# Optimization experiments

Hardware: AMD Instinct MI355X
Metric: run time of the kernel (lower is better)

## Reference

```python
import jax, jax.numpy as jnp
import numpy as np

H, D, K, FF = 8, 512, 64, 64  # n_head, feature_dim, key_feature_dim, dim_feedforward
L, B = 512, 32
LN_EPS = 1e-5


def _l2norm(x, eps=1e-12):
    # torch F.normalize: x / max(||x||, eps)
    n = jnp.sqrt(jnp.sum(x * x, axis=-1, keepdims=True))
    return x / jnp.maximum(n, eps)


def _layernorm(x, g, b, eps=LN_EPS):
    m = jnp.mean(x, axis=-1, keepdims=True)
    v = jnp.mean((x - m) ** 2, axis=-1, keepdims=True)
    return (x - m) * jax.lax.rsqrt(v + eps) * g + b


def setup_inputs() -> dict:
    key0 = jax.random.key(0)
    ks = jax.random.split(key0, 13)
    n = jax.random.normal
    s_kq = float(np.sqrt(2.0 / K))
    s_v = float(np.sqrt(2.0 / D))
    return {
        "query": n(ks[0], (L, B, D), jnp.float32),
        "key": n(ks[1], (L, B, D), jnp.float32),
        "value": n(ks[2], (L, B, D), jnp.float32),
        "WK": n(ks[3], (H, K, D), jnp.float32) * s_kq,
        "WQ": n(ks[4], (H, K, D), jnp.float32) * s_kq,
        "WV": n(ks[5], (H, D, D), jnp.float32) * s_v,
        "Wt": n(ks[6], (H, D, D), jnp.float32) * 0.04,  # trans_conv (default kaiming-ish scale)
        "W1": n(ks[7], (H, FF, D), jnp.float32) * 0.04,
        "b1": jnp.zeros((H, FF), jnp.float32),
        "W2": n(ks[8], (H, D, FF), jnp.float32) * 0.1,
        "b2": jnp.zeros((H, D), jnp.float32),
        "ln_g": jnp.ones((H, D), jnp.float32),
        "ln_b": jnp.zeros((H, D), jnp.float32),
    }


def reference(query, key, value, WK, WQ, WV, Wt, W1, b1, W2, b2, ln_g, ln_b):
    # query/key/value: [L, B, D]; per-head weights stacked on leading H axis.
    Lq, Bb, Dd = query.shape
    Hh = WK.shape[0]

    # per-head cosine-normalized Q/K projections: [H, B, L, K]
    wq = _l2norm(jnp.einsum('lbd,hkd->hblk', query, WQ))
    wk = _l2norm(jnp.einsum('lbd,hkd->hblk', key, WK))

    # attention scores [H, B, Lq, Lk], temp = 1
    dot = jnp.einsum('hbqc,hbkc->hbqk', wq, wk)
    aff = jax.nn.softmax(dot, axis=-1)
    # custom renorm: divide by column sums over the QUERY axis
    aff = aff / (1e-9 + jnp.sum(aff, axis=2, keepdims=True))

    wv = jnp.einsum('lbd,hed->hble', value, WV)        # [H, B, Lk, D]
    out = jnp.einsum('hbqk,hbke->hbqe', aff, wv)       # [H, B, Lq, D]
    out = jnp.transpose(out, (0, 2, 1, 3))             # [H, L, B, D]

    # residual-style trans_conv(query - out) -> relu
    o = jax.nn.relu(jnp.einsum('hlbd,hed->hlbe', query[None] - out, Wt))

    # TransNonlinear FFN (dropout = identity at eval)
    hff = jax.nn.relu(jnp.einsum('hlbd,hfd->hlbf', o, W1) + b1[:, None, None, :])
    s2 = jnp.einsum('hlbf,hdf->hlbd', hff, W2) + b2[:, None, None, :]
    x = _layernorm(o + s2, ln_g[:, None, None, :], ln_b[:, None, None, :])

    # concat heads on last dim, head 0 first: [L, B, H*D]
    return jnp.transpose(x, (1, 2, 0, 3)).reshape(Lq, Bb, Hh * Dd)
```

## Files before the change

### kernel.cpp

```cpp
#include <hip/hip_runtime.h>
#include <stdint.h>

#define HH 8
#define DDIM 512
#define KHEAD 64
#define FFD 64
#define LLEN 512
#define BBATCH 32
#define NTOK 16384

typedef unsigned short u16;
typedef __attribute__((ext_vector_type(8))) __bf16 bf16x8;
typedef __attribute__((ext_vector_type(4))) float f32x4;

__device__ __forceinline__ float bf2f(u16 u) {
    union { uint32_t i; float f; } v; v.i = ((uint32_t)u) << 16; return v.f;
}
__device__ __forceinline__ u16 f2bf(float f) {
    union { uint32_t i; float f; } v; v.f = f;
    return (u16)((v.i + 0x7FFFu + ((v.i >> 16) & 1u)) >> 16);
}

__device__ __forceinline__ void gload16(const void* g, void* l) {
    __builtin_amdgcn_global_load_lds(
        (const __attribute__((address_space(1))) void*)g,
        (__attribute__((address_space(3))) void*)l, 16, 0, 0);
}

__global__ __launch_bounds__(256) void f2bf4(const float* __restrict__ in,
                                             u16* __restrict__ out, int n4) {
    int i = blockIdx.x * 256 + threadIdx.x;
    if (i >= n4) return;
    float4 v = ((const float4*)in)[i];
    ushort4 o; o.x = f2bf(v.x); o.y = f2bf(v.y); o.z = f2bf(v.z); o.w = f2bf(v.w);
    ((ushort4*)out)[i] = o;
}

enum { M_PLAIN = 0, M_WQK = 1, M_SUBAUX = 2, M_RELU = 3, M_ADDAUX = 4, M_SCALECOL = 5 };

template<int BM, int BN, int MODE, int ZMAP, int SWAPXY>
__global__ __launch_bounds__(256) void mgemm(
    const u16* __restrict__ A, const u16* __restrict__ B, u16* __restrict__ C,
    int Kd, int lda, int ldb, int ldc,
    long Ash, long Asb, long Bsh, long Bsb, long Csh, long Csb, int nB2,
    const float* __restrict__ bias, int biasN,
    const void* __restrict__ auxp, long auxsh, long auxsb, int auxld)
{
    constexpr int WC = (BN == 128) ? 2 : 1;
    constexpr int WR = 4 / WC;
    constexpr int WTM = BM / WR;
    constexpr int WTN = BN / WC;
    constexpr int MF = WTM / 16;
    constexpr int NF = WTN / 16;
    constexpr int NCA = (BM * 64) / 4096;
    constexpr int NCB = (BN * 64) / 4096;
    __shared__ u16 As[BM * 32];
    __shared__ u16 Bs[BN * 32];

    const int z = blockIdx.z;
    int h2, b2;
    if (ZMAP == 0)      { h2 = z / nB2;      b2 = z % nB2; }
    else if (ZMAP == 1) { h2 = z & 7;        b2 = z >> 3; }
    else                { h2 = (z >> 3) & 7; b2 = ((z >> 6) << 3) | (z & 7); }
    const u16* Ab = A + h2 * Ash + b2 * Asb;
    const u16* Bb = B + h2 * Bsh + b2 * Bsb;
    const int bx = SWAPXY ? blockIdx.y : blockIdx.x;
    const int by = SWAPXY ? blockIdx.x : blockIdx.y;
    const int m0 = bx * BM, n0 = by * BN;
    const int t = threadIdx.x;
    const int lane = t & 63;
    const int w = t >> 6;
    const int wr = w / WC, wc = w % WC;
    const int tb = t * 16;
    const int wb = (t & 192) * 16;

    f32x4 acc[MF][NF];
    #pragma unroll
    for (int m = 0; m < MF; ++m)
        #pragma unroll
        for (int n = 0; n < NF; ++n)
            #pragma unroll
            for (int i = 0; i < 4; ++i) acc[m][n][i] = 0.f;

    const int ko = (lane >> 4) * 16;

    for (int k0 = 0; k0 < Kd; k0 += 32) {
        #pragma unroll
        for (int c = 0; c < NCA; ++c) {
            const int byte = c * 4096 + tb;
            const int row = byte >> 6;
            gload16((const char*)(Ab + (long)(m0 + row) * lda + k0) + (byte & 63),
                    (char*)As + c * 4096 + wb);
        }
        #pragma unroll
        for (int c = 0; c < NCB; ++c) {
            const int byte = c * 4096 + tb;
            const int row = byte >> 6;
            gload16((const char*)(Bb + (long)(n0 + row) * ldb + k0) + (byte & 63),
                    (char*)Bs + c * 4096 + wb);
        }
        __syncthreads();
        bf16x8 af[MF], bfr[NF];
        #pragma unroll
        for (int m = 0; m < MF; ++m)
            af[m] = *(const bf16x8*)((const char*)As + (wr * WTM + m * 16 + (lane & 15)) * 64 + ko);
        #pragma unroll
        for (int n = 0; n < NF; ++n)
            bfr[n] = *(const bf16x8*)((const char*)Bs + (wc * WTN + n * 16 + (lane & 15)) * 64 + ko);
        #pragma unroll
        for (int m = 0; m < MF; ++m)
            #pragma unroll
            for (int n = 0; n < NF; ++n)
                acc[m][n] = __builtin_amdgcn_mfma_f32_16x16x32_bf16(af[m], bfr[n], acc[m][n], 0, 0, 0);
        __syncthreads();
    }

    const int lr = (lane >> 4) * 4;
    const int lc = lane & 15;

    if constexpr (MODE == M_WQK) {
        const int h = (n0 + wc * WTN) >> 6;
        #pragma unroll
        for (int m = 0; m < MF; ++m) {
            #pragma unroll
            for (int i = 0; i < 4; ++i) {
                float s = 0.f;
                #pragma unroll
                for (int n = 0; n < NF; ++n) { const float v = acc[m][n][i]; s += v * v; }
                s += __shfl_xor(s, 1); s += __shfl_xor(s, 2);
                s += __shfl_xor(s, 4); s += __shfl_xor(s, 8);
                const float inv = 1.0f / fmaxf(sqrtf(s), 1e-12f);
                const int r = m0 + wr * WTM + m * 16 + lr + i;
                const int l = r >> 5, bq = r & 31;
                const int sw = (l & 7) << 3;
                u16* rowp = C + (((long)(h * BBATCH + bq) * LLEN + l) * KHEAD);
                #pragma unroll
                for (int n = 0; n < NF; ++n)
                    rowp[(lc + n * 16) ^ sw] = f2bf(acc[m][n][i] * inv);
            }
        }
    } else {
        const long cof = h2 * Csh + b2 * Csb;
        #pragma unroll
        for (int m = 0; m < MF; ++m) {
            #pragma unroll
            for (int i = 0; i < 4; ++i) {
                const int r = m0 + wr * WTM + m * 16 + lr + i;
                #pragma unroll
                for (int n = 0; n < NF; ++n) {
                    const int c = n0 + wc * WTN + n * 16 + lc;
                    float v = acc[m][n][i];
                    if (MODE == M_SUBAUX) {
                        const u16* q = (const u16*)auxp;
                        v = bf2f(q[auxsh * h2 + auxsb * b2 + (long)r * auxld + c]) - v;
                    } else if (MODE == M_RELU) {
                        if (bias) v += bias[h2 * biasN + c];
                        v = fmaxf(v, 0.0f);
                    } else if (MODE == M_ADDAUX) {
                        v += bias[h2 * biasN + c];
                        const u16* ax = (const u16*)auxp;
                        v += bf2f(ax[auxsh * h2 + auxsb * b2 + (long)r * auxld + c]);
                    } else if (MODE == M_SCALECOL) {
                        const float* cs = (const float*)auxp + auxsh * h2 + auxsb * b2;
                        v *= 1.0f / (1e-9f + cs[c]);
                    }
                    C[cof + (long)r * ldc + c] = f2bf(v);
                }
            }
        }
    }
}

__global__ __launch_bounds__(256) void attn_mfma(
    const u16* __restrict__ wq, const u16* __restrict__ wk,
    u16* __restrict__ P, float* __restrict__ colsum)
{
    __shared__ u16 qs[64 * 64];
    __shared__ u16 ks[512 * 64];
    __shared__ float smax[4][64];
    __shared__ float ssum[4][64];

    const int qt = blockIdx.x, b = blockIdx.y, h = blockIdx.z;
    const long hb = h * BBATCH + b;
    const int t = threadIdx.x;
    const int lane = t & 63, w = t >> 6;
    const int wb = (t & 192) * 16;

    const char* qg = (const char*)(wq + (hb * LLEN + qt * 64) * KHEAD);
    const char* kg = (const char*)(wk + hb * LLEN * KHEAD);
    #pragma unroll
    for (int c = 0; c < 2; ++c)
        gload16(qg + c * 4096 + t * 16, (char*)qs + c * 4096 + wb);
    #pragma unroll
    for (int c = 0; c < 16; ++c)
        gload16(kg + c * 4096 + t * 16, (char*)ks + c * 4096 + wb);
    __syncthreads();

    const int l15 = lane & 15;
    const int g = lane >> 4;
    const int swz = (lane & 7) << 4;

    f32x4 acc[4][8];
    #pragma unroll
    for (int m = 0; m < 4; ++m)
        #pragma unroll
        for (int n = 0; n < 8; ++n)
            #pragma unroll
            for (int i = 0; i < 4; ++i) acc[m][n][i] = 0.f;

    #pragma unroll
    for (int kk = 0; kk < 2; ++kk) {
        bf16x8 af[4];
        #pragma unroll
        for (int m = 0; m < 4; ++m) {
            const int row = m * 16 + l15;
            af[m] = *(const bf16x8*)((const char*)qs + row * 128 + ((g * 16 + kk * 64) ^ swz));
        }
        #pragma unroll
        for (int n = 0; n < 8; ++n) {
            const int row = (w * 8 + n) * 16 + l15;
            const bf16x8 bfr = *(const bf16x8*)((const char*)ks + row * 128 + ((g * 16 + kk * 64) ^ swz));
            #pragma unroll
            for (int m = 0; m < 4; ++m)
                acc[m][n] = __builtin_amdgcn_mfma_f32_16x16x32_bf16(af[m], bfr, acc[m][n], 0, 0, 0);
        }
    }

    float rmax[4][4];
    #pragma unroll
    for (int m = 0; m < 4; ++m)
        #pragma unroll
        for (int i = 0; i < 4; ++i) {
            float mx = acc[m][0][i];
            #pragma unroll
            for (int n = 1; n < 8; ++n) mx = fmaxf(mx, acc[m][n][i]);
            mx = fmaxf(mx, __shfl_xor(mx, 1));
            mx = fmaxf(mx, __shfl_xor(mx, 2));
            mx = fmaxf(mx, __shfl_xor(mx, 4));
            mx = fmaxf(mx, __shfl_xor(mx, 8));
            if (l15 == 0) smax[w][m * 16 + g * 4 + i] = mx;
        }
    __syncthreads();
    #pragma unroll
    for (int m = 0; m < 4; ++m)
        #pragma unroll
        for (int i = 0; i < 4; ++i) {
            const int r = m * 16 + g * 4 + i;
            rmax[m][i] = fmaxf(fmaxf(smax[0][r], smax[1][r]),
                               fmaxf(smax[2][r], smax[3][r]));
        }
    float rinv[4][4];
    #pragma unroll
    for (int m = 0; m < 4; ++m)
        #pragma unroll
        for (int i = 0; i < 4; ++i) {
            float s = 0.f;
            #pragma unroll
            for (int n = 0; n < 8; ++n) {
                acc[m][n][i] = __expf(acc[m][n][i] - rmax[m][i]);
                s += acc[m][n][i];
            }
            s += __shfl_xor(s, 1); s += __shfl_xor(s, 2);
            s += __shfl_xor(s, 4); s += __shfl_xor(s, 8);
            if (l15 == 0) ssum[w][m * 16 + g * 4 + i] = s;
        }
    __syncthreads();
    #pragma unroll
    for (int m = 0; m < 4; ++m)
        #pragma unroll
        for (int i = 0; i < 4; ++i) {
            const int r = m * 16 + g * 4 + i;
            rinv[m][i] = 1.0f / (ssum[0][r] + ssum[1][r] + ssum[2][r] + ssum[3][r]);
        }

    u16* Pb = P + (hb * LLEN + qt * 64) * LLEN + w * 128;
    float cs[8];
    #pragma unroll
    for (int n = 0; n < 8; ++n) cs[n] = 0.f;
    #pragma unroll
    for (int m = 0; m < 4; ++m)
        #pragma unroll
        for (int i = 0; i < 4; ++i) {
            const int r = m * 16 + g * 4 + i;
            u16* pr = Pb + (long)r * LLEN + l15;
            const float iv = rinv[m][i];
            #pragma unroll
            for (int n = 0; n < 8; ++n) {
                const float p = acc[m][n][i] * iv;
                pr[n * 16] = f2bf(p);
                cs[n] += p;
            }
        }
    #pragma unroll
    for (int n = 0; n < 8; ++n) {
        cs[n] += __shfl_xor(cs[n], 16);
        cs[n] += __shfl_xor(cs[n], 32);
    }
    if (lane < 16) {
        float* cb = colsum + hb * 512 + w * 128 + lane;
        #pragma unroll
        for (int n = 0; n < 8; ++n) atomicAdd(&cb[n * 16], cs[n]);
    }
}

__global__ __launch_bounds__(256) void ln_out(
    const u16* __restrict__ x, const float* __restrict__ g,
    const float* __restrict__ bb, float* __restrict__ out)
{
    const int t = threadIdx.x;
    const int w = t >> 6, lane = t & 63;
    const long row = (long)blockIdx.x * 4 + w;
    const int h = (int)(row >> 14);
    const int t2 = (int)(row & 16383);
    const int b = t2 >> 9, l = t2 & 511;
    const u16* xp = x + row * DDIM;
    float v[8];
    float s = 0.f, sq = 0.f;
    #pragma unroll
    for (int j = 0; j < 8; ++j) {
        v[j] = bf2f(xp[j * 64 + lane]);
        s += v[j]; sq += v[j] * v[j];
    }
    #pragma unroll
    for (int off = 32; off >= 1; off >>= 1) {
        s += __shfl_xor(s, off);
        sq += __shfl_xor(sq, off);
    }
    const float mean = s * (1.0f / 512.0f);
    const float var = sq * (1.0f / 512.0f) - mean * mean;
    const float rs = rsqrtf(var + 1e-5f);
    const float* gp = g + h * DDIM;
    const float* bp = bb + h * DDIM;
    float* op = out + ((long)l * BBATCH + b) * (HH * DDIM) + h * DDIM;
    #pragma unroll
    for (int j = 0; j < 8; ++j) {
        const int d = j * 64 + lane;
        op[d] = (v[j] - mean) * rs * gp[d] + bp[d];
    }
}

extern "C" void kernel_launch(void* const* d_in, const int* in_sizes, int n_in,
                              void* d_out, int out_size, void* d_ws, size_t ws_size,
                              hipStream_t stream) {
    const float* query = (const float*)d_in[0];
    const float* key   = (const float*)d_in[1];
    const float* value = (const float*)d_in[2];
    const float* WK = (const float*)d_in[3];
    const float* WQ = (const float*)d_in[4];
    const float* WV = (const float*)d_in[5];
    const float* Wt = (const float*)d_in[6];
    const float* W1 = (const float*)d_in[7];
    const float* b1 = (const float*)d_in[8];
    const float* W2 = (const float*)d_in[9];
    const float* b2 = (const float*)d_in[10];
    const float* lng = (const float*)d_in[11];
    const float* lnb = (const float*)d_in[12];

    char* ws = (char*)d_ws;
    u16* kbf  = (u16*)(ws);
    u16* WQbf = (u16*)(ws + 16777216);
    u16* WKbf = (u16*)(ws + 17301504);
    u16* P    = (u16*)(ws);
    u16* preLN = P;
    u16* vbf  = (u16*)(ws + 134217728);
    u16* WVbf = (u16*)(ws + 150994944);
    u16* o    = (u16*)(ws + 134217728);
    float* colsum = (float*)(ws + 268435456);
    u16* qbf  = (u16*)(ws + 268959744);
    u16* hff  = qbf;
    u16* wq   = (u16*)(ws + 285736960);
    u16* wk   = (u16*)(ws + 302514176);
    u16* Wtbf = (u16*)(ws + 285736960);
    u16* W1bf = (u16*)(ws + 289931264);
    u16* W2bf = (u16*)(ws + 290455552);
    u16* qmo = (u16*)d_out;
    u16* wvT = (u16*)((char*)d_out + 134217728);

    if (ws_size < 319291392u) return;

    hipMemsetAsync(colsum, 0, 524288, stream);
    const dim3 blk(256);

    f2bf4<<<dim3(8192), blk, 0, stream>>>(query, qbf, 2097152);
    f2bf4<<<dim3(8192), blk, 0, stream>>>(key,   kbf, 2097152);
    f2bf4<<<dim3(8192), blk, 0, stream>>>(value, vbf, 2097152);
    f2bf4<<<dim3(256),  blk, 0, stream>>>(WQ, WQbf, 65536);
    f2bf4<<<dim3(256),  blk, 0, stream>>>(WK, WKbf, 65536);
    f2bf4<<<dim3(2048), blk, 0, stream>>>(WV, WVbf, 524288);

    mgemm<128, 128, M_WQK, 0, 1><<<dim3(4, 128, 1), blk, 0, stream>>>(
        qbf, WQbf, wq, 512, 512, 512, 0,
        0, 0, 0, 0, 0, 0, 1, nullptr, 0, nullptr, 0, 0, 0);
    mgemm<128, 128, M_WQK, 0, 1><<<dim3(4, 128, 1), blk, 0, stream>>>(
        kbf, WKbf, wk, 512, 512, 512, 0,
        0, 0, 0, 0, 0, 0, 1, nullptr, 0, nullptr, 0, 0, 0);

    attn_mfma<<<dim3(8, 32, 8), blk, 0, stream>>>(wq, wk, P, colsum);

    f2bf4<<<dim3(2048), blk, 0, stream>>>(Wt, Wtbf, 524288);
    f2bf4<<<dim3(256),  blk, 0, stream>>>(W1, W1bf, 65536);
    f2bf4<<<dim3(256),  blk, 0, stream>>>(W2, W2bf, 65536);

    mgemm<128, 128, M_SCALECOL, 2, 0><<<dim3(4, 4, 256), blk, 0, stream>>>(
        WVbf, vbf, wvT, 512, 512, BBATCH * DDIM, 512,
        (long)DDIM * DDIM, 0, 0, DDIM,
        (long)BBATCH * DDIM * LLEN, (long)DDIM * LLEN, 32,
        nullptr, 0, colsum, (long)BBATCH * 512, 512, 0);

    mgemm<128, 128, M_SUBAUX, 1, 0><<<dim3(4, 4, 256), blk, 0, stream>>>(
        P, wvT, qmo, 512, 512, 512, 512,
        (long)BBATCH * LLEN * LLEN, (long)LLEN * LLEN,
        (long)BBATCH * DDIM * LLEN, (long)DDIM * LLEN,
        (long)BBATCH * LLEN * DDIM, (long)LLEN * DDIM, 32,
        nullptr, 0, qbf, 0, DDIM, BBATCH * DDIM);

    mgemm<128, 128, M_RELU, 0, 1><<<dim3(4, 128, 8), blk, 0, stream>>>(
        qmo, Wtbf, o, 512, 512, 512, 512,
        (long)NTOK * DDIM, 0, (long)DDIM * DDIM, 0,
        (long)NTOK * DDIM, 0, 1, nullptr, 512, nullptr, 0, 0, 0);

    mgemm<128, 64, M_RELU, 0, 0><<<dim3(128, 1, 8), blk, 0, stream>>>(
        o, W1bf, hff, 512, 512, 512, 64,
        (long)NTOK * DDIM, 0, (long)FFD * DDIM, 0,
        (long)NTOK * FFD, 0, 1, b1, 64, nullptr, 0, 0, 0);

    mgemm<128, 128, M_ADDAUX, 0, 1><<<dim3(4, 128, 8), blk, 0, stream>>>(
        hff, W2bf, preLN, 64, 64, 64, 512,
        (long)NTOK * FFD, 0, (long)DDIM * FFD, 0,
        (long)NTOK * DDIM, 0, 1, b2, 512, o, (long)NTOK * DDIM, 0, 512);

    ln_out<<<dim3(32768), blk, 0, stream>>>(preLN, lng, lnb, (float*)d_out);
}
```

Baseline: 803.4 us.

## Double-buffer GEMM LDS tiles and fuse FFN second GEMM with LayerNorm

The generic GEMM now keeps two LDS buffers and issues the next K-slice's global-to-LDS loads before computing on the current one, aiming to hide load latency behind MFMA work. The W2 projection, bias, residual add and LayerNorm are merged into one kernel. It keeps W2 for a head in LDS and reduces row statistics across waves, which removes the bf16 preLN round-trip and a separate launch. In exchange the kernels use more LDS (64KB W2 tile plus double buffers), which may lower occupancy. The fused kernel also reads the residual from global memory with an uncoalesced per-fragment pattern.

```diff
diff --git a/kernel.cpp b/kernel.cpp
--- a/kernel.cpp
+++ b/kernel.cpp
@@ -54,8 +54,8 @@
     constexpr int NF = WTN / 16;
     constexpr int NCA = (BM * 64) / 4096;
     constexpr int NCB = (BN * 64) / 4096;
-    __shared__ u16 As[BM * 32];
-    __shared__ u16 Bs[BN * 32];
+    __shared__ u16 As[2][BM * 32];
+    __shared__ u16 Bs[2][BN * 32];
 
     const int z = blockIdx.z;
     int h2, b2;
@@ -84,35 +84,43 @@
 
     const int ko = (lane >> 4) * 16;
 
-    for (int k0 = 0; k0 < Kd; k0 += 32) {
+    auto stage = [&](int buf, int k0) {
         #pragma unroll
         for (int c = 0; c < NCA; ++c) {
             const int byte = c * 4096 + tb;
             const int row = byte >> 6;
             gload16((const char*)(Ab + (long)(m0 + row) * lda + k0) + (byte & 63),
-                    (char*)As + c * 4096 + wb);
+                    (char*)As[buf] + c * 4096 + wb);
         }
         #pragma unroll
         for (int c = 0; c < NCB; ++c) {
             const int byte = c * 4096 + tb;
             const int row = byte >> 6;
             gload16((const char*)(Bb + (long)(n0 + row) * ldb + k0) + (byte & 63),
-                    (char*)Bs + c * 4096 + wb);
-        }
-        __syncthreads();
+                    (char*)Bs[buf] + c * 4096 + wb);
+        }
+    };
+
+    stage(0, 0);
+    __syncthreads();
+    int cur = 0;
+    const int nsteps = Kd >> 5;
+    for (int s = 0; s < nsteps; ++s) {
+        if (s + 1 < nsteps) stage(cur ^ 1, (s + 1) << 5);
         bf16x8 af[MF], bfr[NF];
         #pragma unroll
         for (int m = 0; m < MF; ++m)
-            af[m] = *(const bf16x8*)((const char*)As + (wr * WTM + m * 16 + (lane & 15)) * 64 + ko);
+            af[m] = *(const bf16x8*)((const char*)As[cur] + (wr * WTM + m * 16 + (lane & 15)) * 64 + ko);
         #pragma unroll
         for (int n = 0; n < NF; ++n)
-            bfr[n] = *(const bf16x8*)((const char*)Bs + (wc * WTN + n * 16 + (lane & 15)) * 64 + ko);
+            bfr[n] = *(const bf16x8*)((const char*)Bs[cur] + (wc * WTN + n * 16 + (lane & 15)) * 64 + ko);
         #pragma unroll
         for (int m = 0; m < MF; ++m)
             #pragma unroll
             for (int n = 0; n < NF; ++n)
                 acc[m][n] = __builtin_amdgcn_mfma_f32_16x16x32_bf16(af[m], bfr[n], acc[m][n], 0, 0, 0);
         __syncthreads();
+        cur ^= 1;
     }
 
     const int lr = (lane >> 4) * 4;
@@ -303,40 +311,104 @@
     }
 }
 
-__global__ __launch_bounds__(256) void ln_out(
-    const u16* __restrict__ x, const float* __restrict__ g,
-    const float* __restrict__ bb, float* __restrict__ out)
+__global__ __launch_bounds__(256) void ffn2_ln(
+    const u16* __restrict__ hff, const u16* __restrict__ W2bf,
+    const float* __restrict__ b2, const u16* __restrict__ o,
+    const float* __restrict__ lng, const float* __restrict__ lnb,
+    float* __restrict__ out)
 {
+    __shared__ u16 W2s[512 * 64];
+    __shared__ u16 hs[32 * 64];
+    __shared__ float redS[4][32];
+    __shared__ float redQ[4][32];
+
+    const int h = blockIdx.z;
+    const int m0 = blockIdx.x * 32;
     const int t = threadIdx.x;
-    const int w = t >> 6, lane = t & 63;
-    const long row = (long)blockIdx.x * 4 + w;
-    const int h = (int)(row >> 14);
-    const int t2 = (int)(row & 16383);
-    const int b = t2 >> 9, l = t2 & 511;
-    const u16* xp = x + row * DDIM;
-    float v[8];
-    float s = 0.f, sq = 0.f;
-    #pragma unroll
-    for (int j = 0; j < 8; ++j) {
-        v[j] = bf2f(xp[j * 64 + lane]);
-        s += v[j]; sq += v[j] * v[j];
-    }
-    #pragma unroll
-    for (int off = 32; off >= 1; off >>= 1) {
-        s += __shfl_xor(s, off);
-        sq += __shfl_xor(sq, off);
-    }
-    const float mean = s * (1.0f / 512.0f);
-    const float var = sq * (1.0f / 512.0f) - mean * mean;
-    const float rs = rsqrtf(var + 1e-5f);
-    const float* gp = g + h * DDIM;
-    const float* bp = bb + h * DDIM;
-    float* op = out + ((long)l * BBATCH + b) * (HH * DDIM) + h * DDIM;
-    #pragma unroll
-    for (int j = 0; j < 8; ++j) {
-        const int d = j * 64 + lane;
-        op[d] = (v[j] - mean) * rs * gp[d] + bp[d];
-    }
+    const int lane = t & 63, w = t >> 6;
+    const int l15 = lane & 15, g = lane >> 4;
+    const int wb = (t & 192) * 16;
+
+    const char* w2g = (const char*)W2bf + (long)h * 65536;
+    #pragma unroll
+    for (int c = 0; c < 16; ++c)
+        gload16(w2g + c * 4096 + t * 16, (char*)W2s + c * 4096 + wb);
+    gload16((const char*)hff + ((long)h * NTOK + m0) * 128 + t * 16, (char*)hs + wb);
+    __syncthreads();
+
+    f32x4 acc[2][8];
+    #pragma unroll
+    for (int m = 0; m < 2; ++m)
+        #pragma unroll
+        for (int n = 0; n < 8; ++n)
+            #pragma unroll
+            for (int i = 0; i < 4; ++i) acc[m][n][i] = 0.f;
+
+    #pragma unroll
+    for (int kk = 0; kk < 2; ++kk) {
+        bf16x8 af[2];
+        #pragma unroll
+        for (int m = 0; m < 2; ++m)
+            af[m] = *(const bf16x8*)((const char*)hs + (m * 16 + l15) * 128 + kk * 64 + g * 16);
+        #pragma unroll
+        for (int n = 0; n < 8; ++n) {
+            const int e = w * 128 + n * 16 + l15;
+            const bf16x8 bfr = *(const bf16x8*)((const char*)W2s + e * 128 + kk * 64 + g * 16);
+            #pragma unroll
+            for (int m = 0; m < 2; ++m)
+                acc[m][n] = __builtin_amdgcn_mfma_f32_16x16x32_bf16(af[m], bfr, acc[m][n], 0, 0, 0);
+        }
+    }
+
+    float b2v[8], gv[8], bv[8];
+    #pragma unroll
+    for (int n = 0; n < 8; ++n) {
+        const int c = w * 128 + n * 16 + l15;
+        b2v[n] = b2[h * DDIM + c];
+        gv[n] = lng[h * DDIM + c];
+        bv[n] = lnb[h * DDIM + c];
+    }
+    const u16* ob = o + ((long)h * NTOK + m0) * DDIM;
+    #pragma unroll
+    for (int m = 0; m < 2; ++m)
+        #pragma unroll
+        for (int i = 0; i < 4; ++i) {
+            const int row = m * 16 + g * 4 + i;
+            float s = 0.f, q = 0.f;
+            #pragma unroll
+            for (int n = 0; n < 8; ++n) {
+                const int c = w * 128 + n * 16 + l15;
+                const float v = acc[m][n][i] + b2v[n] + bf2f(ob[(long)row * DDIM + c]);
+                acc[m][n][i] = v;
+                s += v; q += v * v;
+            }
+            s += __shfl_xor(s, 1); q += __shfl_xor(q, 1);
+            s += __shfl_xor(s, 2); q += __shfl_xor(q, 2);
+            s += __shfl_xor(s, 4); q += __shfl_xor(q, 4);
+            s += __shfl_xor(s, 8); q += __shfl_xor(q, 8);
+            if (l15 == 0) { redS[w][row] = s; redQ[w][row] = q; }
+        }
+    __syncthreads();
+
+    #pragma unroll
+    for (int m = 0; m < 2; ++m)
+        #pragma unroll
+        for (int i = 0; i < 4; ++i) {
+            const int row = m * 16 + g * 4 + i;
+            const float s = redS[0][row] + redS[1][row] + redS[2][row] + redS[3][row];
+            const float q = redQ[0][row] + redQ[1][row] + redQ[2][row] + redQ[3][row];
+            const float mu = s * (1.0f / 512.0f);
+            const float var = q * (1.0f / 512.0f) - mu * mu;
+            const float rs = rsqrtf(var + 1e-5f);
+            const int tok = m0 + row;
+            const int b = tok >> 9, l = tok & 511;
+            float* op = out + ((long)(l * BBATCH + b)) * (HH * DDIM) + h * DDIM;
+            #pragma unroll
+            for (int n = 0; n < 8; ++n) {
+                const int c = w * 128 + n * 16 + l15;
+                op[c] = (acc[m][n][i] - mu) * rs * gv[n] + bv[n];
+            }
+        }
 }
 
 extern "C" void kernel_launch(void* const* d_in, const int* in_sizes, int n_in,
@@ -361,7 +433,6 @@
     u16* WQbf = (u16*)(ws + 16777216);
     u16* WKbf = (u16*)(ws + 17301504);
     u16* P    = (u16*)(ws);
-    u16* preLN = P;
     u16* vbf  = (u16*)(ws + 134217728);
     u16* WVbf = (u16*)(ws + 150994944);
     u16* o    = (u16*)(ws + 134217728);
@@ -424,10 +495,6 @@
         (long)NTOK * DDIM, 0, (long)FFD * DDIM, 0,
         (long)NTOK * FFD, 0, 1, b1, 64, nullptr, 0, 0, 0);
 
-    mgemm<128, 128, M_ADDAUX, 0, 1><<<dim3(4, 128, 8), blk, 0, stream>>>(
-        hff, W2bf, preLN, 64, 64, 64, 512,
-        (long)NTOK * FFD, 0, (long)DDIM * FFD, 0,
-        (long)NTOK * DDIM, 0, 1, b2, 512, o, (long)NTOK * DDIM, 0, 512);
-
-    ln_out<<<dim3(32768), blk, 0, stream>>>(preLN, lng, lnb, (float*)d_out);
-}
+    ffn2_ln<<<dim3(512, 1, 8), blk, 0, stream>>>(hff, W2bf, b2, o, lng, lnb,
+                                                 (float*)d_out);
+}
```

New measurement: 771.8 us. 3.9% less time.
